# Performance work log

Hardware: AMD Instinct MI355X
Metric: run time of the kernel (lower is better)

The kernel has to match this reference:

```python
import jax, jax.numpy as jnp
import numpy as np
from jax import lax

B, S, L = 128, 256, 10
WORD, CHAR = 50000, 100
TAGS, START, END = 32, 30, 31
WDIM, CDIM, FILT, H = 100, 30, 30, 100
LSTM_IN = WDIM + FILT  # 130
NEG = -10000.0


def setup_inputs() -> dict:
    key = jax.random.key(0)
    ks = jax.random.split(key, 24)
    sc = 0.1
    word_emb = (jax.random.normal(ks[0], (WORD, WDIM), jnp.float32) * sc).at[0].set(0.0)  # padding_idx=0
    char_emb = (jax.random.normal(ks[1], (CHAR, CDIM), jnp.float32) * sc).at[0].set(0.0)
    conv_w = jax.random.normal(ks[2], (FILT, 1, 3, CDIM), jnp.float32) * sc  # OIHW, kernel (3, char_dim)
    conv_b = jax.random.normal(ks[3], (FILT,), jnp.float32) * sc
    wih_f = jax.random.normal(ks[4], (4 * H, LSTM_IN), jnp.float32) * sc
    whh_f = jax.random.normal(ks[5], (4 * H, H), jnp.float32) * sc
    bih_f = jax.random.normal(ks[6], (4 * H,), jnp.float32) * sc
    bhh_f = jax.random.normal(ks[7], (4 * H,), jnp.float32) * sc
    wih_b = jax.random.normal(ks[8], (4 * H, LSTM_IN), jnp.float32) * sc
    whh_b = jax.random.normal(ks[9], (4 * H, H), jnp.float32) * sc
    bih_b = jax.random.normal(ks[10], (4 * H,), jnp.float32) * sc
    bhh_b = jax.random.normal(ks[11], (4 * H,), jnp.float32) * sc
    proj_w = jax.random.normal(ks[12], (TAGS, 2 * H), jnp.float32) * sc
    proj_b = jax.random.normal(ks[13], (TAGS,), jnp.float32) * sc
    trans = jax.random.normal(ks[14], (TAGS, TAGS), jnp.float32)
    trans = trans.at[:, START].set(NEG).at[END, :].set(NEG)  # CRF.reset_parm
    word_x = jax.random.randint(ks[15], (B, S), 1, WORD, jnp.int32)
    char_x = jax.random.randint(ks[16], (B, S, L), 1, CHAR, jnp.int32)
    y = jax.random.randint(ks[17], (B, S), 0, 30, jnp.int32)  # gold tags exclude start/end
    mask = jnp.ones((B, S), jnp.int32)
    return dict(word_emb=word_emb, char_emb=char_emb, conv_w=conv_w, conv_b=conv_b,
                wih_f=wih_f, whh_f=whh_f, bih_f=bih_f, bhh_f=bhh_f,
                wih_b=wih_b, whh_b=whh_b, bih_b=bih_b, bhh_b=bhh_b,
                proj_w=proj_w, proj_b=proj_b, trans=trans,
                word_x=word_x, char_x=char_x, y=y, mask=mask)


def _lstm_dir(x, wih, whh, bih, bhh, reverse):
    # x: [B, S, D] -> hidden states [B, S, H]; PyTorch gate order i, f, g, o
    b = bih + bhh
    xs = jnp.swapaxes(x, 0, 1)  # [S, B, D]
    if reverse:
        xs = xs[::-1]
    Bv = x.shape[0]
    Hd = whh.shape[1]
    init = (jnp.zeros((Bv, Hd), x.dtype), jnp.zeros((Bv, Hd), x.dtype))
    def step(carry, xt):
        h, c = carry
        g = xt @ wih.T + h @ whh.T + b  # [B, 4H]
        i, f, gg, o = jnp.split(g, 4, axis=-1)
        c = jax.nn.sigmoid(f) * c + jax.nn.sigmoid(i) * jnp.tanh(gg)
        h = jax.nn.sigmoid(o) * jnp.tanh(c)
        return (h, c), h
    _, hs = lax.scan(step, init, xs)
    if reverse:
        hs = hs[::-1]
    return jnp.swapaxes(hs, 0, 1)


def _forward(word_emb, char_emb, conv_w, conv_b, wih_f, whh_f, bih_f, bhh_f,
             wih_b, whh_b, bih_b, bhh_b, proj_w, proj_b, trans,
             word_x, char_x, y, mask):
    # --- CharCNN (dropout = identity in eval) ---
    ce = char_emb[char_x].reshape(B * S, 1, L, CDIM)  # [B*S, 1, L, CDIM]
    fm = lax.conv_general_dilated(ce, conv_w, (1, 1), ((2, 2), (0, 0)),
                                  dimension_numbers=('NCHW', 'OIHW', 'NCHW'))
    fm = fm + conv_b[None, :, None, None]  # [B*S, FILT, L+2, 1]
    char_feat = fm.max(axis=(2, 3)).reshape(B, S, FILT)
    # --- BiLSTM + projection ---
    x = jnp.concatenate([word_emb[word_x], char_feat], axis=-1)  # [B, S, 130]
    h_f = _lstm_dir(x, wih_f, whh_f, bih_f, bhh_f, False)
    h_b = _lstm_dir(x, wih_b, whh_b, bih_b, bhh_b, True)
    emission = jnp.concatenate([h_f, h_b], axis=-1) @ proj_w.T + proj_b  # [B, S, TAGS]
    maskf = mask.astype(emission.dtype)
    # --- CRF gold-path score (vectorized form of compute_y_score) ---
    y_pad = jnp.concatenate([jnp.full((B, 1), START, y.dtype), y], axis=1)  # [B, S+1]
    prev, cur = y_pad[:, :-1], y_pad[:, 1:]
    p = jnp.take_along_axis(emission, cur[..., None].astype(jnp.int32), axis=-1)[..., 0]
    t = trans[prev, cur]
    score_y = ((p + t) * maskf).sum(axis=1) + trans[y[:, -1], END]  # original uses last label unmasked
    # --- CRF partition function (logsumexp scan over time) ---
    la0 = jnp.full((B, TAGS), NEG, emission.dtype).at[:, START].set(0.0)
    def step(la, em_m):
        em, m = em_m  # em: [B, TAGS], m: [B]
        la2 = jax.nn.logsumexp(la[:, :, None] + trans[None, :, :] + em[:, None, :], axis=1)
        m = m[:, None]
        return la2 * m + la * (1.0 - m), None
    la, _ = lax.scan(step, la0, (jnp.swapaxes(emission, 0, 1), maskf.T))
    la = la + trans[:, END][None, :]
    total = jax.nn.logsumexp(la, axis=1, keepdims=True)  # [B, 1]
    # faithful to original: [B] - [B,1] broadcasts to [B,B], then mean
    return -jnp.mean(score_y - total)


def reference(word_emb, char_emb, conv_w, conv_b, wih_f, whh_f, bih_f, bhh_f,
              wih_b, whh_b, bih_b, bhh_b, proj_w, proj_b, trans,
              word_x, char_x, y, mask):
    return _forward(word_emb, char_emb, conv_w, conv_b, wih_f, whh_f, bih_f, bhh_f,
                    wih_b, whh_b, bih_b, bhh_b, proj_w, proj_b, trans,
                    word_x, char_x, y, mask)
```

## Files before the change

kernel.cpp:

```cpp
#include <hip/hip_runtime.h>
#include <hip/hip_fp16.h>
#include <cstdint>
#include <cstddef>

#define BB 128
#define SS 256
#define LL 10
#define NTAGS 32
#define TAG_START 30
#define TAG_END 31
#define WDIM 100
#define CDIM 30
#define NFILT 30
#define HDIM 100
#define KIN 130
#define KPAD 160
#define GDIM 400
#define NROWS 832
#define NEGV -10000.0f
#define CTOK 8

#define NB_CONV (BB * SS / CTOK)
#define NB_WORD (BB * SS * KPAD / 256)
#define NB_WCVT (NROWS * KPAD / 256)
#define NB_PRE  (NB_CONV + NB_WORD + NB_WCVT)

typedef _Float16 h2 __attribute__((ext_vector_type(2)));
typedef _Float16 f16x8 __attribute__((ext_vector_type(8)));
typedef float f32x4 __attribute__((ext_vector_type(4)));

__device__ __forceinline__ float sigm(float x) { return 1.0f / (1.0f + __expf(-x)); }
__device__ __forceinline__ float tanh_fast(float x) { return 2.0f / (1.0f + __expf(-2.0f * x)) - 1.0f; }

__device__ __forceinline__ void barrier_lds_only() {
  asm volatile("s_waitcnt lgkmcnt(0)" ::: "memory");
  __builtin_amdgcn_s_barrier();
  asm volatile("" ::: "memory");
}

__global__ __launch_bounds__(256) void k_pre(
    const float* __restrict__ wemb, const int* __restrict__ wx,
    const float* __restrict__ cemb, const float* __restrict__ convw,
    const float* __restrict__ convb, const int* __restrict__ cx,
    const float* __restrict__ wihF, const float* __restrict__ wihB,
    _Float16* __restrict__ x16, _Float16* __restrict__ w16,
    float* __restrict__ out) {
  int blk = blockIdx.x;
  int tid = threadIdx.x;
  if (blk == 0 && tid == 0) out[0] = 0.f;

  if (blk < NB_CONV) {
    int tok8 = tid >> 5;
    int f = tid & 31;
    int token0 = blk * CTOK;
    __shared__ float e[CTOK][LL * CDIM];
    __shared__ float cw[NFILT * 3 * CDIM];
    __shared__ float cb[NFILT];
    __shared__ int ci[CTOK][LL];
    if (tid < CTOK * LL) {
      int t = tid / LL, l = tid - t * LL;
      ci[t][l] = cx[(token0 + t) * LL + l];
    }
    for (int i = tid; i < NFILT * 3 * CDIM; i += 256) cw[i] = convw[i];
    if (tid < NFILT) cb[tid] = convb[tid];
    __syncthreads();
    for (int i = tid; i < CTOK * LL * CDIM; i += 256) {
      int t = i / (LL * CDIM);
      int r = i - t * (LL * CDIM);
      int l = r / CDIM, c = r - l * CDIM;
      e[t][l * CDIM + c] = cemb[ci[t][l] * CDIM + c];
    }
    __syncthreads();
    if (f < NFILT) {
      float d0[LL], d1[LL], d2[LL];
#pragma unroll
      for (int l = 0; l < LL; l++) { d0[l] = 0.f; d1[l] = 0.f; d2[l] = 0.f; }
      const float* et = &e[tok8][0];
      for (int c = 0; c < CDIM; c++) {
        float w0 = cw[(f * 3 + 0) * CDIM + c];
        float w1 = cw[(f * 3 + 1) * CDIM + c];
        float w2 = cw[(f * 3 + 2) * CDIM + c];
#pragma unroll
        for (int l = 0; l < LL; l++) {
          float ev = et[l * CDIM + c];
          d0[l] += ev * w0; d1[l] += ev * w1; d2[l] += ev * w2;
        }
      }
      float bias = cb[f];
      float m = -3.0e38f;
#pragma unroll
      for (int h = 0; h < LL + 2; h++) {
        float acc = bias;
        int j0 = h - 2, j1 = h - 1, j2 = h;
        if (j0 >= 0 && j0 < LL) acc += d0[j0];
        if (j1 >= 0 && j1 < LL) acc += d1[j1];
        if (j2 >= 0 && j2 < LL) acc += d2[j2];
        m = fmaxf(m, acc);
      }
      x16[(size_t)(token0 + tok8) * KPAD + WDIM + f] = (_Float16)m;
    }
  } else if (blk < NB_CONV + NB_WORD) {
    int idx = (blk - NB_CONV) * 256 + tid;
    int token = idx / KPAD;
    int d = idx - token * KPAD;
    if (d < WDIM) {
      x16[idx] = (_Float16)wemb[(size_t)wx[token] * WDIM + d];
    } else if (d >= KIN) {
      x16[idx] = (_Float16)0.f;
    }
  } else {
    int idx = (blk - NB_CONV - NB_WORD) * 256 + tid;
    int n = idx / KPAD;
    int k = idx - n * KPAD;
    float v = 0.f;
    if (k < KIN && n < 2 * GDIM) {
      v = (n < GDIM) ? wihF[(size_t)n * KIN + k] : wihB[(size_t)(n - GDIM) * KIN + k];
    }
    w16[idx] = (_Float16)v;
  }
}

__global__ __launch_bounds__(256) void k_pregemm(
    const _Float16* __restrict__ x16, const _Float16* __restrict__ w16,
    const float* __restrict__ bihF, const float* __restrict__ bhhF,
    const float* __restrict__ bihB, const float* __restrict__ bhhB,
    _Float16* __restrict__ preF, _Float16* __restrict__ preB) {
  __shared__ __align__(16) _Float16 Asl[64 * 40];
  __shared__ __align__(16) _Float16 Bsl[64 * 40];
  int m0 = blockIdx.x * 64;
  int n0 = blockIdx.y * 64;
  int tid = threadIdx.x;
  int lane = tid & 63, w = tid >> 6;
  int quad = lane >> 4, l15 = lane & 15;

  f32x4 acc[4];
#pragma unroll
  for (int i = 0; i < 4; i++) acc[i] = (f32x4){0.f, 0.f, 0.f, 0.f};

  int r = tid >> 2;
  int kk = (tid & 3) * 8;
  const _Float16* xs = x16 + (size_t)(m0 + r) * KPAD + kk;
  const _Float16* wsrc = w16 + (size_t)(n0 + r) * KPAD + kk;

  for (int kc = 0; kc < 5; kc++) {
    if (kc) __syncthreads();
    *(f16x8*)&Asl[r * 40 + kk] = *(const f16x8*)(xs + kc * 32);
    *(f16x8*)&Bsl[r * 40 + kk] = *(const f16x8*)(wsrc + kc * 32);
    __syncthreads();

    f16x8 bfrag = *(const f16x8*)&Bsl[(w * 16 + l15) * 40 + quad * 8];
#pragma unroll
    for (int mt = 0; mt < 4; mt++) {
      f16x8 afrag = *(const f16x8*)&Asl[(mt * 16 + l15) * 40 + quad * 8];
      acc[mt] = __builtin_amdgcn_mfma_f32_16x16x32_f16(afrag, bfrag, acc[mt], 0, 0, 0);
    }
  }

  int ng = n0 + w * 16 + l15;
  if (ng < 2 * GDIM) {
    int dir = ng >= GDIM;
    int jb = dir ? ng - GDIM : ng;
    _Float16* dst = dir ? preB : preF;
    float bias = (dir ? bihB : bihF)[jb] + (dir ? bhhB : bhhF)[jb];
#pragma unroll
    for (int mt = 0; mt < 4; mt++) {
#pragma unroll
      for (int i = 0; i < 4; i++) {
        int m = m0 + mt * 16 + quad * 4 + i;
        dst[(size_t)m * GDIM + jb] = (_Float16)(acc[mt][i] + bias);
      }
    }
  }
}

__global__ __launch_bounds__(256, 1) void k_lstm(
    const _Float16* __restrict__ preF, const _Float16* __restrict__ preB,
    const float* __restrict__ whhF, const float* __restrict__ whhB,
    _Float16* __restrict__ hbuf) {
  int blk = blockIdx.x;
  int dir = blk >> 7;
  int b = blk & 127;
  const _Float16* pre = dir ? preB : preF;
  const float* whh = dir ? whhB : whhF;
  int tid = threadIdx.x;
  int j = tid >> 1;
  int kh = tid & 1;
  bool act = (j < HDIM);
  int jc = act ? j : 0;

  __half2 wp[4][25];
#pragma unroll
  for (int g = 0; g < 4; g++) {
    const float* wr = whh + (size_t)(g * HDIM + jc) * HDIM + kh * 50;
#pragma unroll
    for (int q = 0; q < 25; q++) {
      wp[g][q] = __floats2half2_rn(wr[2 * q], wr[2 * q + 1]);
    }
  }

  __shared__ __align__(16) _Float16 hsh[2][2][64];
  if (tid < 128) ((int*)hsh)[tid] = 0;
  float c = 0.f;

  int t0 = dir ? (SS - 1) : 0;
  const intptr_t pstep = dir ? -(intptr_t)GDIM : (intptr_t)GDIM;
  const _Float16* pbase = pre + ((size_t)b * SS + t0) * GDIM + kh * 200 + jc;
  _Float16 pa0 = pbase[0], pb0 = pbase[100];
  _Float16 pa1 = pbase[pstep], pb1 = pbase[pstep + 100];
  __syncthreads();

  int cur = 0;
  for (int s = 0; s < SS; s++) {
    int sn = (s + 2 < SS) ? (s + 2) : (SS - 1);
    const _Float16* pn = pbase + (intptr_t)sn * pstep;
    _Float16 pa2 = pn[0], pb2 = pn[100];

    const _Float16* hseg = &hsh[cur][kh][0];
    uint4 hv0 = *(const uint4*)(hseg);
    uint4 hv1 = *(const uint4*)(hseg + 8);
    uint4 hv2 = *(const uint4*)(hseg + 16);
    uint4 hv3 = *(const uint4*)(hseg + 24);
    uint4 hv4 = *(const uint4*)(hseg + 32);
    uint4 hv5 = *(const uint4*)(hseg + 40);
    uint32_t hv6 = *(const uint32_t*)(hseg + 48);
    __half2 hp[25];
    hp[0]  = __builtin_bit_cast(__half2, hv0.x);
    hp[1]  = __builtin_bit_cast(__half2, hv0.y);
    hp[2]  = __builtin_bit_cast(__half2, hv0.z);
    hp[3]  = __builtin_bit_cast(__half2, hv0.w);
    hp[4]  = __builtin_bit_cast(__half2, hv1.x);
    hp[5]  = __builtin_bit_cast(__half2, hv1.y);
    hp[6]  = __builtin_bit_cast(__half2, hv1.z);
    hp[7]  = __builtin_bit_cast(__half2, hv1.w);
    hp[8]  = __builtin_bit_cast(__half2, hv2.x);
    hp[9]  = __builtin_bit_cast(__half2, hv2.y);
    hp[10] = __builtin_bit_cast(__half2, hv2.z);
    hp[11] = __builtin_bit_cast(__half2, hv2.w);
    hp[12] = __builtin_bit_cast(__half2, hv3.x);
    hp[13] = __builtin_bit_cast(__half2, hv3.y);
    hp[14] = __builtin_bit_cast(__half2, hv3.z);
    hp[15] = __builtin_bit_cast(__half2, hv3.w);
    hp[16] = __builtin_bit_cast(__half2, hv4.x);
    hp[17] = __builtin_bit_cast(__half2, hv4.y);
    hp[18] = __builtin_bit_cast(__half2, hv4.z);
    hp[19] = __builtin_bit_cast(__half2, hv4.w);
    hp[20] = __builtin_bit_cast(__half2, hv5.x);
    hp[21] = __builtin_bit_cast(__half2, hv5.y);
    hp[22] = __builtin_bit_cast(__half2, hv5.z);
    hp[23] = __builtin_bit_cast(__half2, hv5.w);
    hp[24] = __builtin_bit_cast(__half2, hv6);

    float racc[4];
    __half2 z = __floats2half2_rn(0.f, 0.f);
#pragma unroll
    for (int g = 0; g < 4; g++) {
      __half2 a0 = z, a1 = z;
#pragma unroll
      for (int q = 0; q < 25; q += 2) a0 = __hfma2(wp[g][q], hp[q], a0);
#pragma unroll
      for (int q = 1; q < 25; q += 2) a1 = __hfma2(wp[g][q], hp[q], a1);
      racc[g] = (__low2float(a0) + __high2float(a0)) +
                (__low2float(a1) + __high2float(a1));
    }

    if (kh == 0) { racc[0] += (float)pa0; racc[1] += (float)pb0; }
    else         { racc[2] += (float)pa0; racc[3] += (float)pb0; }
#pragma unroll
    for (int g = 0; g < 4; g++) racc[g] += __shfl_xor(racc[g], 1);

    float ig = sigm(racc[0]), fg = sigm(racc[1]);
    float g2 = tanh_fast(racc[2]), og = sigm(racc[3]);
    c = fg * c + ig * g2;
    float h = og * tanh_fast(c);

    if (act && kh == 0) {
      int seg = (j >= 50) ? 1 : 0;
      hsh[cur ^ 1][seg][j - seg * 50] = (_Float16)h;
      int t = dir ? (SS - 1 - s) : s;
      hbuf[((size_t)b * SS + t) * (2 * HDIM) + dir * HDIM + j] = (_Float16)h;
    }

    barrier_lds_only();
    cur ^= 1;
    pa0 = pa1; pb0 = pb1; pa1 = pa2; pb1 = pb2;
  }
}

__global__ __launch_bounds__(256) void k_proj(const _Float16* __restrict__ hbuf,
                                              const float* __restrict__ pw,
                                              const float* __restrict__ pb,
                                              float* __restrict__ em) {
  __shared__ __align__(16) float pws[NTAGS * 204];
  __shared__ float pbs[NTAGS];
  int tid = threadIdx.x;
  for (int i = tid; i < NTAGS * 2 * HDIM; i += 256) {
    int tag = i / (2 * HDIM);
    int k = i - tag * (2 * HDIM);
    pws[tag * 204 + k] = pw[i];
  }
  if (tid < NTAGS) pbs[tid] = pb[tid];
  __syncthreads();

  int idx = blockIdx.x * blockDim.x + tid;
  if (idx >= BB * SS * NTAGS) return;
  int token = idx >> 5, tag = idx & 31;
  const uint4* h4 = (const uint4*)(hbuf + (size_t)token * 2 * HDIM);
  const float4* w4 = (const float4*)&pws[tag * 204];
  float acc = pbs[tag];
#pragma unroll
  for (int k = 0; k < 25; k++) {
    uint4 hv = h4[k];
    h2 a = __builtin_bit_cast(h2, hv.x);
    h2 bq = __builtin_bit_cast(h2, hv.y);
    h2 cq = __builtin_bit_cast(h2, hv.z);
    h2 d = __builtin_bit_cast(h2, hv.w);
    float4 w0 = w4[k * 2], w1 = w4[k * 2 + 1];
    acc += (float)a.x * w0.x + (float)a.y * w0.y + (float)bq.x * w0.z + (float)bq.y * w0.w
         + (float)cq.x * w1.x + (float)cq.y * w1.y + (float)d.x * w1.z + (float)d.y * w1.w;
  }
  em[idx] = acc;
}

__global__ __launch_bounds__(64) void k_crf(const float* __restrict__ em,
                                            const float* __restrict__ trans,
                                            const int* __restrict__ mask,
                                            const int* __restrict__ y,
                                            float* __restrict__ out) {
  int b = blockIdx.x;
  int lane = threadIdx.x;
  int j = lane & 31;
  int h = lane >> 5;

  float sacc = 0.f;
  for (int s = lane; s < SS; s += 64) {
    int curt = y[b * SS + s];
    int prevt = (s == 0) ? TAG_START : y[b * SS + s - 1];
    float mk = (float)mask[b * SS + s];
    sacc += (em[((size_t)b * SS + s) * NTAGS + curt] + trans[prevt * NTAGS + curt]) * mk;
  }
#pragma unroll
  for (int off = 32; off > 0; off >>= 1) sacc += __shfl_down(sacc, off);
  float scoreYv = __shfl(sacc, 0) + trans[y[b * SS + SS - 1] * NTAGS + TAG_END];

  float tcol[16];
#pragma unroll
  for (int i = 0; i < 16; i++) tcol[i] = trans[(h * 16 + i) * NTAGS + j];

  float la = (j == TAG_START) ? 0.f : NEGV;

  const float* emb = em + (size_t)b * SS * NTAGS + j;
  const int* mkb = mask + b * SS;
  float e0 = emb[0], e1 = emb[NTAGS];
  int m0i = mkb[0], m1i = mkb[1];

  for (int s = 0; s < SS; s++) {
    int sn = (s + 2 < SS) ? (s + 2) : (SS - 1);
    float e2 = emb[(size_t)sn * NTAGS];
    int m2i = mkb[sn];

    float v[16];
#pragma unroll
    for (int i = 0; i < 16; i++) v[i] = __shfl(la, h * 16 + i) + tcol[i];

    float ma = v[0], mb2 = v[1];
#pragma unroll
    for (int i = 2; i < 16; i += 2) { ma = fmaxf(ma, v[i]); mb2 = fmaxf(mb2, v[i + 1]); }
    float mh = fmaxf(ma, mb2);
    float m = fmaxf(mh, __shfl_xor(mh, 32));

    float sa = 0.f, sb = 0.f;
#pragma unroll
    for (int i = 0; i < 16; i += 2) { sa += __expf(v[i] - m); sb += __expf(v[i + 1] - m); }
    float sh = sa + sb;
    float sum = sh + __shfl_xor(sh, 32);

    float la2 = m + __logf(sum) + e0;
    float mk = (float)m0i;
    la = la2 * mk + la * (1.f - mk);
    e0 = e1; e1 = e2; m0i = m1i; m1i = m2i;
  }
  la += trans[j * NTAGS + TAG_END];

  float mm = la;
#pragma unroll
  for (int off = 16; off > 0; off >>= 1) mm = fmaxf(mm, __shfl_xor(mm, off));
  float ss = __expf(la - mm);
#pragma unroll
  for (int off = 16; off > 0; off >>= 1) ss += __shfl_xor(ss, off);
  float total = mm + __logf(ss);
  if (lane == 0) atomicAdd(out, (total - scoreYv) * (1.0f / BB));
}

extern "C" void kernel_launch(void* const* d_in, const int* in_sizes, int n_in,
                              void* d_out, int out_size, void* d_ws, size_t ws_size,
                              hipStream_t stream) {
  const float* word_emb = (const float*)d_in[0];
  const float* char_emb = (const float*)d_in[1];
  const float* conv_w   = (const float*)d_in[2];
  const float* conv_b   = (const float*)d_in[3];
  const float* wih_f    = (const float*)d_in[4];
  const float* whh_f    = (const float*)d_in[5];
  const float* bih_f    = (const float*)d_in[6];
  const float* bhh_f    = (const float*)d_in[7];
  const float* wih_b    = (const float*)d_in[8];
  const float* whh_b    = (const float*)d_in[9];
  const float* bih_b    = (const float*)d_in[10];
  const float* bhh_b    = (const float*)d_in[11];
  const float* proj_w   = (const float*)d_in[12];
  const float* proj_b   = (const float*)d_in[13];
  const float* trans    = (const float*)d_in[14];
  const int* word_x     = (const int*)d_in[15];
  const int* char_x     = (const int*)d_in[16];
  const int* y          = (const int*)d_in[17];
  const int* mask       = (const int*)d_in[18];
  float* out = (float*)d_out;

  _Float16* x16   = (_Float16*)d_ws;
  _Float16* w16   = x16 + (size_t)BB * SS * KPAD;
  _Float16* preF  = w16 + (size_t)NROWS * KPAD;
  _Float16* preB  = preF + (size_t)BB * SS * GDIM;
  _Float16* hbuf  = preB + (size_t)BB * SS * GDIM;
  float* em       = (float*)(hbuf + (size_t)BB * SS * 2 * HDIM);

  k_pre<<<NB_PRE, 256, 0, stream>>>(word_emb, word_x, char_emb, conv_w, conv_b,
                                    char_x, wih_f, wih_b, x16, w16, out);
  k_pregemm<<<dim3(BB * SS / 64, 13), 256, 0, stream>>>(x16, w16, bih_f, bhh_f,
                                                        bih_b, bhh_b, preF, preB);
  k_lstm<<<256, 256, 0, stream>>>(preF, preB, whh_f, whh_b, hbuf);
  k_proj<<<(BB * SS * NTAGS + 255) / 256, 256, 0, stream>>>(hbuf, proj_w, proj_b, em);
  k_crf<<<BB, 64, 0, stream>>>(em, trans, mask, y, out);
}
```

Before: 537.4 us.

## Stage LSTM preactivations in LDS chunks, use fdot2, and stage CRF emissions

```diff
diff --git a/kernel.cpp b/kernel.cpp
--- a/kernel.cpp
+++ b/kernel.cpp
@@ -29,6 +29,12 @@
 typedef _Float16 f16x8 __attribute__((ext_vector_type(8)));
 typedef float f32x4 __attribute__((ext_vector_type(4)));
 
+#if __has_builtin(__builtin_amdgcn_fdot2)
+#define HAVE_FDOT2 1
+#else
+#define HAVE_FDOT2 0
+#endif
+
 __device__ __forceinline__ float sigm(float x) { return 1.0f / (1.0f + __expf(-x)); }
 __device__ __forceinline__ float tanh_fast(float x) { return 2.0f / (1.0f + __expf(-2.0f * x)) - 1.0f; }
 
@@ -173,6 +179,8 @@
   }
 }
 
+#define CH 32
+#define NCH (SS / CH)
 __global__ __launch_bounds__(256, 1) void k_lstm(
     const _Float16* __restrict__ preF, const _Float16* __restrict__ preB,
     const float* __restrict__ whhF, const float* __restrict__ whhB,
@@ -198,92 +206,136 @@
     }
   }
 
+  __shared__ __align__(16) _Float16 preS[14336];
   __shared__ __align__(16) _Float16 hsh[2][2][64];
   if (tid < 128) ((int*)hsh)[tid] = 0;
   float c = 0.f;
 
-  int t0 = dir ? (SS - 1) : 0;
-  const intptr_t pstep = dir ? -(intptr_t)GDIM : (intptr_t)GDIM;
-  const _Float16* pbase = pre + ((size_t)b * SS + t0) * GDIM + kh * 200 + jc;
-  _Float16 pa0 = pbase[0], pb0 = pbase[100];
-  _Float16 pa1 = pbase[pstep], pb1 = pbase[pstep + 100];
-  __syncthreads();
+#define GSRC(ck) ((const uint4*)(pre + ((size_t)b * SS + (dir ? (SS - CH - (ck) * CH) : ((ck) * CH))) * GDIM))
+
+  uint4 r0, r1, r2, r3, r4, r5, r6;
+  {
+    const uint4* s0 = GSRC(0);
+    r0 = s0[0 * 256 + tid]; r1 = s0[1 * 256 + tid]; r2 = s0[2 * 256 + tid];
+    r3 = s0[3 * 256 + tid]; r4 = s0[4 * 256 + tid]; r5 = s0[5 * 256 + tid];
+    r6 = s0[6 * 256 + tid];
+  }
+
+  _Float16* hptr = hbuf + ((size_t)b * SS + (dir ? (SS - 1) : 0)) * (2 * HDIM) + dir * HDIM + jc;
+  const intptr_t hstep = dir ? -(intptr_t)(2 * HDIM) : (intptr_t)(2 * HDIM);
 
   int cur = 0;
-  for (int s = 0; s < SS; s++) {
-    int sn = (s + 2 < SS) ? (s + 2) : (SS - 1);
-    const _Float16* pn = pbase + (intptr_t)sn * pstep;
-    _Float16 pa2 = pn[0], pb2 = pn[100];
-
-    const _Float16* hseg = &hsh[cur][kh][0];
-    uint4 hv0 = *(const uint4*)(hseg);
-    uint4 hv1 = *(const uint4*)(hseg + 8);
-    uint4 hv2 = *(const uint4*)(hseg + 16);
-    uint4 hv3 = *(const uint4*)(hseg + 24);
-    uint4 hv4 = *(const uint4*)(hseg + 32);
-    uint4 hv5 = *(const uint4*)(hseg + 40);
-    uint32_t hv6 = *(const uint32_t*)(hseg + 48);
-    __half2 hp[25];
-    hp[0]  = __builtin_bit_cast(__half2, hv0.x);
-    hp[1]  = __builtin_bit_cast(__half2, hv0.y);
-    hp[2]  = __builtin_bit_cast(__half2, hv0.z);
-    hp[3]  = __builtin_bit_cast(__half2, hv0.w);
-    hp[4]  = __builtin_bit_cast(__half2, hv1.x);
-    hp[5]  = __builtin_bit_cast(__half2, hv1.y);
-    hp[6]  = __builtin_bit_cast(__half2, hv1.z);
-    hp[7]  = __builtin_bit_cast(__half2, hv1.w);
-    hp[8]  = __builtin_bit_cast(__half2, hv2.x);
-    hp[9]  = __builtin_bit_cast(__half2, hv2.y);
-    hp[10] = __builtin_bit_cast(__half2, hv2.z);
-    hp[11] = __builtin_bit_cast(__half2, hv2.w);
-    hp[12] = __builtin_bit_cast(__half2, hv3.x);
-    hp[13] = __builtin_bit_cast(__half2, hv3.y);
-    hp[14] = __builtin_bit_cast(__half2, hv3.z);
-    hp[15] = __builtin_bit_cast(__half2, hv3.w);
-    hp[16] = __builtin_bit_cast(__half2, hv4.x);
-    hp[17] = __builtin_bit_cast(__half2, hv4.y);
-    hp[18] = __builtin_bit_cast(__half2, hv4.z);
-    hp[19] = __builtin_bit_cast(__half2, hv4.w);
-    hp[20] = __builtin_bit_cast(__half2, hv5.x);
-    hp[21] = __builtin_bit_cast(__half2, hv5.y);
-    hp[22] = __builtin_bit_cast(__half2, hv5.z);
-    hp[23] = __builtin_bit_cast(__half2, hv5.w);
-    hp[24] = __builtin_bit_cast(__half2, hv6);
-
-    float racc[4];
-    __half2 z = __floats2half2_rn(0.f, 0.f);
-#pragma unroll
-    for (int g = 0; g < 4; g++) {
-      __half2 a0 = z, a1 = z;
-#pragma unroll
-      for (int q = 0; q < 25; q += 2) a0 = __hfma2(wp[g][q], hp[q], a0);
-#pragma unroll
-      for (int q = 1; q < 25; q += 2) a1 = __hfma2(wp[g][q], hp[q], a1);
-      racc[g] = (__low2float(a0) + __high2float(a0)) +
-                (__low2float(a1) + __high2float(a1));
-    }
-
-    if (kh == 0) { racc[0] += (float)pa0; racc[1] += (float)pb0; }
-    else         { racc[2] += (float)pa0; racc[3] += (float)pb0; }
-#pragma unroll
-    for (int g = 0; g < 4; g++) racc[g] += __shfl_xor(racc[g], 1);
-
-    float ig = sigm(racc[0]), fg = sigm(racc[1]);
-    float g2 = tanh_fast(racc[2]), og = sigm(racc[3]);
-    c = fg * c + ig * g2;
-    float h = og * tanh_fast(c);
-
-    if (act && kh == 0) {
-      int seg = (j >= 50) ? 1 : 0;
-      hsh[cur ^ 1][seg][j - seg * 50] = (_Float16)h;
-      int t = dir ? (SS - 1 - s) : s;
-      hbuf[((size_t)b * SS + t) * (2 * HDIM) + dir * HDIM + j] = (_Float16)h;
-    }
-
+  for (int ck = 0; ck < NCH; ck++) {
+    asm volatile("s_waitcnt vmcnt(0)" ::: "memory");
+    *(uint4*)&preS[(0 * 256 + tid) * 8] = r0;
+    *(uint4*)&preS[(1 * 256 + tid) * 8] = r1;
+    *(uint4*)&preS[(2 * 256 + tid) * 8] = r2;
+    *(uint4*)&preS[(3 * 256 + tid) * 8] = r3;
+    *(uint4*)&preS[(4 * 256 + tid) * 8] = r4;
+    *(uint4*)&preS[(5 * 256 + tid) * 8] = r5;
+    *(uint4*)&preS[(6 * 256 + tid) * 8] = r6;
+    if (ck + 1 < NCH) {
+      const uint4* snx = GSRC(ck + 1);
+      r0 = snx[0 * 256 + tid]; r1 = snx[1 * 256 + tid]; r2 = snx[2 * 256 + tid];
+      r3 = snx[3 * 256 + tid]; r4 = snx[4 * 256 + tid]; r5 = snx[5 * 256 + tid];
+      r6 = snx[6 * 256 + tid];
+    }
     barrier_lds_only();
-    cur ^= 1;
-    pa0 = pa1; pb0 = pb1; pa1 = pa2; pb1 = pb2;
-  }
+
+    int preOff = (dir ? (CH - 1) * GDIM : 0) + kh * 200 + jc;
+    const int pdelta = dir ? -GDIM : GDIM;
+
+    for (int s2 = 0; s2 < CH; s2++) {
+      float paF = (float)preS[preOff];
+      float pbF = (float)preS[preOff + 100];
+
+      const _Float16* hseg = &hsh[cur][kh][0];
+      uint4 hv0 = *(const uint4*)(hseg);
+      uint4 hv1 = *(const uint4*)(hseg + 8);
+      uint4 hv2 = *(const uint4*)(hseg + 16);
+      uint4 hv3 = *(const uint4*)(hseg + 24);
+      uint4 hv4 = *(const uint4*)(hseg + 32);
+      uint4 hv5 = *(const uint4*)(hseg + 40);
+      uint32_t hv6 = *(const uint32_t*)(hseg + 48);
+      __half2 hp[25];
+      hp[0]  = __builtin_bit_cast(__half2, hv0.x);
+      hp[1]  = __builtin_bit_cast(__half2, hv0.y);
+      hp[2]  = __builtin_bit_cast(__half2, hv0.z);
+      hp[3]  = __builtin_bit_cast(__half2, hv0.w);
+      hp[4]  = __builtin_bit_cast(__half2, hv1.x);
+      hp[5]  = __builtin_bit_cast(__half2, hv1.y);
+      hp[6]  = __builtin_bit_cast(__half2, hv1.z);
+      hp[7]  = __builtin_bit_cast(__half2, hv1.w);
+      hp[8]  = __builtin_bit_cast(__half2, hv2.x);
+      hp[9]  = __builtin_bit_cast(__half2, hv2.y);
+      hp[10] = __builtin_bit_cast(__half2, hv2.z);
+      hp[11] = __builtin_bit_cast(__half2, hv2.w);
+      hp[12] = __builtin_bit_cast(__half2, hv3.x);
+      hp[13] = __builtin_bit_cast(__half2, hv3.y);
+      hp[14] = __builtin_bit_cast(__half2, hv3.z);
+      hp[15] = __builtin_bit_cast(__half2, hv3.w);
+      hp[16] = __builtin_bit_cast(__half2, hv4.x);
+      hp[17] = __builtin_bit_cast(__half2, hv4.y);
+      hp[18] = __builtin_bit_cast(__half2, hv4.z);
+      hp[19] = __builtin_bit_cast(__half2, hv4.w);
+      hp[20] = __builtin_bit_cast(__half2, hv5.x);
+      hp[21] = __builtin_bit_cast(__half2, hv5.y);
+      hp[22] = __builtin_bit_cast(__half2, hv5.z);
+      hp[23] = __builtin_bit_cast(__half2, hv5.w);
+      hp[24] = __builtin_bit_cast(__half2, hv6);
+
+      float racc[4];
+#if HAVE_FDOT2
+#pragma unroll
+      for (int g = 0; g < 4; g++) {
+        float a0 = 0.f, a1 = 0.f;
+#pragma unroll
+        for (int q = 0; q < 25; q += 2)
+          a0 = __builtin_amdgcn_fdot2(__builtin_bit_cast(h2, wp[g][q]),
+                                      __builtin_bit_cast(h2, hp[q]), a0, false);
+#pragma unroll
+        for (int q = 1; q < 25; q += 2)
+          a1 = __builtin_amdgcn_fdot2(__builtin_bit_cast(h2, wp[g][q]),
+                                      __builtin_bit_cast(h2, hp[q]), a1, false);
+        racc[g] = a0 + a1;
+      }
+#else
+      __half2 z = __floats2half2_rn(0.f, 0.f);
+#pragma unroll
+      for (int g = 0; g < 4; g++) {
+        __half2 a0 = z, a1 = z;
+#pragma unroll
+        for (int q = 0; q < 25; q += 2) a0 = __hfma2(wp[g][q], hp[q], a0);
+#pragma unroll
+        for (int q = 1; q < 25; q += 2) a1 = __hfma2(wp[g][q], hp[q], a1);
+        racc[g] = (__low2float(a0) + __high2float(a0)) +
+                  (__low2float(a1) + __high2float(a1));
+      }
+#endif
+
+      if (kh == 0) { racc[0] += paF; racc[1] += pbF; }
+      else         { racc[2] += paF; racc[3] += pbF; }
+#pragma unroll
+      for (int g = 0; g < 4; g++) racc[g] += __shfl_xor(racc[g], 1);
+
+      float ig = sigm(racc[0]), fg = sigm(racc[1]);
+      float g2 = tanh_fast(racc[2]), og = sigm(racc[3]);
+      c = fg * c + ig * g2;
+      float h = og * tanh_fast(c);
+
+      if (act && kh == 0) {
+        int seg = (j >= 50) ? 1 : 0;
+        hsh[cur ^ 1][seg][j - seg * 50] = (_Float16)h;
+        *hptr = (_Float16)h;
+      }
+
+      barrier_lds_only();
+      cur ^= 1;
+      preOff += pdelta;
+      hptr += hstep;
+    }
+  }
+#undef GSRC
 }
 
 __global__ __launch_bounds__(256) void k_proj(const _Float16* __restrict__ hbuf,
@@ -331,12 +383,26 @@
   int j = lane & 31;
   int h = lane >> 5;
 
+  __shared__ __align__(16) float emS[SS * NTAGS];
+  __shared__ __align__(16) int mkS[SS];
+  {
+    const uint4* src = (const uint4*)(em + (size_t)b * SS * NTAGS);
+#pragma unroll
+    for (int p = 0; p < 32; p++) {
+      uint4 t = src[p * 64 + lane];
+      *(uint4*)&emS[(p * 64 + lane) * 4] = t;
+    }
+    uint4 mv = ((const uint4*)(mask + (size_t)b * SS))[lane];
+    *(uint4*)&mkS[lane * 4] = mv;
+  }
+  barrier_lds_only();
+
   float sacc = 0.f;
   for (int s = lane; s < SS; s += 64) {
     int curt = y[b * SS + s];
     int prevt = (s == 0) ? TAG_START : y[b * SS + s - 1];
-    float mk = (float)mask[b * SS + s];
-    sacc += (em[((size_t)b * SS + s) * NTAGS + curt] + trans[prevt * NTAGS + curt]) * mk;
+    float mk = (float)mkS[s];
+    sacc += (emS[s * NTAGS + curt] + trans[prevt * NTAGS + curt]) * mk;
   }
 #pragma unroll
   for (int off = 32; off > 0; off >>= 1) sacc += __shfl_down(sacc, off);
@@ -348,15 +414,9 @@
 
   float la = (j == TAG_START) ? 0.f : NEGV;
 
-  const float* emb = em + (size_t)b * SS * NTAGS + j;
-  const int* mkb = mask + b * SS;
-  float e0 = emb[0], e1 = emb[NTAGS];
-  int m0i = mkb[0], m1i = mkb[1];
-
   for (int s = 0; s < SS; s++) {
-    int sn = (s + 2 < SS) ? (s + 2) : (SS - 1);
-    float e2 = emb[(size_t)sn * NTAGS];
-    int m2i = mkb[sn];
+    float e0 = emS[s * NTAGS + j];
+    float mkv = (float)mkS[s];
 
     float v[16];
 #pragma unroll
@@ -375,9 +435,7 @@
     float sum = sh + __shfl_xor(sh, 32);
 
     float la2 = m + __logf(sum) + e0;
-    float mk = (float)m0i;
-    la = la2 * mk + la * (1.f - mk);
-    e0 = e1; e1 = e2; m0i = m1i; m1i = m2i;
+    la = la2 * mkv + la * (1.f - mkv);
   }
   la += trans[j * NTAGS + TAG_END];
 
```

Result: faster. 495.2 us (-7.9%).
